# Kernel tuning notes

Hardware: AMD Instinct MI355X
Metric: run time of the kernel (lower is better)

Reference implementation:

```python
import jax, jax.numpy as jnp
import numpy as np

N_NODES = 200000
N_EDGES = 6400000
D_IN, D_HID, D_OUT = 128, 16, 172


def gcn_conv(x, edge_index, W, b, n):
    """PyG GCNConv: add self-loops, symmetric D^-1/2 A D^-1/2 normalization,
    linear projection, scatter-add aggregation, bias."""
    src, dst = edge_index[0], edge_index[1]
    loops = jnp.arange(n, dtype=edge_index.dtype)
    src = jnp.concatenate([src, loops])
    dst = jnp.concatenate([dst, loops])
    # in-degree with self-loops (>= 1, so rsqrt is safe)
    deg = jax.ops.segment_sum(jnp.ones_like(dst, dtype=x.dtype), dst, num_segments=n)
    dinv = jax.lax.rsqrt(deg)
    lin = x @ W  # [n, d_out]
    norm = dinv[src] * dinv[dst]  # per-edge normalization
    msg = lin[src] * norm[:, None]  # gather + scale
    out = jax.ops.segment_sum(msg, dst, num_segments=n)  # scatter-add
    return out + b


def setup_inputs() -> dict:
    key = jax.random.key(0)
    k1, k2, k3, k4, k5, k6 = jax.random.split(key, 6)
    x = jax.random.normal(k1, (N_NODES, D_IN), dtype=jnp.float32)
    edge_index = jax.random.randint(k2, (2, N_EDGES), 0, N_NODES, dtype=jnp.int64)
    W1 = jax.random.normal(k3, (D_IN, D_HID), dtype=jnp.float32) * (1.0 / np.sqrt(D_IN))
    b1 = jnp.zeros((D_HID,), dtype=jnp.float32)
    W2 = jax.random.normal(k4, (D_HID, D_OUT), dtype=jnp.float32) * (1.0 / np.sqrt(D_HID))
    b2 = jnp.zeros((D_OUT,), dtype=jnp.float32)
    return {"x": x, "edge_index": edge_index, "W1": W1, "b1": b1, "W2": W2, "b2": b2}


def reference(x, edge_index, W1, b1, W2, b2):
    n = x.shape[0]
    # CRD: GCNConv -> relu (dropout is identity in eval mode)
    h = jax.nn.relu(gcn_conv(x, edge_index, W1, b1, n))
    # CLS: GCNConv -> log_softmax over classes
    logits = gcn_conv(h, edge_index, W2, b2, n)
    return jax.nn.log_softmax(logits, axis=1)
```

## Files before the change

### kernel.cpp

```cpp
#include <hip/hip_runtime.h>
#include <hip/hip_fp16.h>

#define N_NODES 200000
#define N_EDGES 6400000
#define D_IN    128
#define D_HID   16
#define D_OUT   172

#define NS1     800
#define EPB     8000
#define SBN     98
#define SB_NODES 2048

#define O_BTOT  0
#define O_BASE  128
#define O_CNT1  256
#define O_ROW   78656
#define O_DINV  278784
#define O_COL   478784
#define O_PACK  6878784
#define O_F16A  6878784
#define O_F16B  8478784
#define O_AGG2  10078784

__global__ __launch_bounds__(256) void k_hist1(const int* __restrict__ dst,
                                               unsigned* __restrict__ counts) {
    __shared__ unsigned cnt[SBN];
    for (int i = threadIdx.x; i < SBN; i += 256) cnt[i] = 0;
    __syncthreads();
    const int* dp = dst + blockIdx.x * EPB;
    for (int i = threadIdx.x; i < EPB; i += 256)
        atomicAdd(&cnt[dp[i] >> 11], 1u);
    __syncthreads();
    unsigned* out = counts + (size_t)blockIdx.x * SBN;
    for (int i = threadIdx.x; i < SBN; i += 256) out[i] = cnt[i];
}

__global__ __launch_bounds__(256) void k_scan_col(unsigned* __restrict__ counts,
                                                  unsigned* __restrict__ btot) {
    __shared__ unsigned arr[NS1];
    int b = blockIdx.x;
    for (int i = threadIdx.x; i < NS1; i += 256)
        arr[i] = counts[(size_t)i * SBN + b];
    __syncthreads();
    if (threadIdx.x < 64) {
        int l = threadIdx.x;
        int lo = l * 13, hi = min(lo + 13, NS1);
        unsigned sum = 0;
        for (int i = lo; i < hi; ++i) sum += arr[i];
        unsigned incl = sum;
#pragma unroll
        for (int o = 1; o < 64; o <<= 1) {
            unsigned tmp = __shfl_up(incl, o);
            if (l >= o) incl += tmp;
        }
        if (l == 63) btot[b] = incl;
        unsigned run = incl - sum;
        for (int i = lo; i < hi; ++i) { unsigned v = arr[i]; arr[i] = run; run += v; }
    }
    __syncthreads();
    for (int i = threadIdx.x; i < NS1; i += 256)
        counts[(size_t)i * SBN + b] = arr[i];
}

__global__ __launch_bounds__(64) void k_scan_base(const unsigned* __restrict__ btot,
                                                  unsigned* __restrict__ base) {
    int l = threadIdx.x;
    int lo = l * 2, hi = min(lo + 2, SBN);
    unsigned sum = 0;
    for (int i = lo; i < hi; ++i) sum += btot[i];
    unsigned incl = sum;
#pragma unroll
    for (int o = 1; o < 64; o <<= 1) {
        unsigned tmp = __shfl_up(incl, o);
        if (l >= o) incl += tmp;
    }
    unsigned run = incl - sum;
    for (int i = lo; i < hi; ++i) { unsigned v = btot[i]; base[i] = run; run += v; }
    if (l == 63) base[SBN] = incl;
}

__global__ __launch_bounds__(256) void k_scatter1(const int* __restrict__ src,
                                                  const int* __restrict__ dst,
                                                  const unsigned* __restrict__ counts,
                                                  const unsigned* __restrict__ base,
                                                  unsigned* __restrict__ packed) {
    __shared__ unsigned off[SBN];
    const unsigned* crow = counts + (size_t)blockIdx.x * SBN;
    for (int i = threadIdx.x; i < SBN; i += 256) off[i] = base[i] + crow[i];
    __syncthreads();
    const int* sp = src + blockIdx.x * EPB;
    const int* dp = dst + blockIdx.x * EPB;
    for (int i = threadIdx.x; i < EPB; i += 256) {
        int s = sp[i], d = dp[i];
        unsigned slot = atomicAdd(&off[d >> 11], 1u);
        packed[slot] = ((unsigned)(d & (SB_NODES - 1)) << 18) | (unsigned)s;
    }
}

__global__ __launch_bounds__(1024) void k_csr(const unsigned* __restrict__ packed,
                                              const unsigned* __restrict__ base,
                                              int* __restrict__ rowptr,
                                              float* __restrict__ dinv,
                                              int* __restrict__ col) {
    __shared__ unsigned cnt[SB_NODES];
    __shared__ unsigned off[SB_NODES];
    __shared__ unsigned wsum[16];
    int t = threadIdx.x, sb = blockIdx.x;
    unsigned beg = base[sb], end = base[sb + 1];
    cnt[t] = 0; cnt[t + 1024] = 0;
    __syncthreads();
    for (unsigned i = beg + t; i < end; i += 1024)
        atomicAdd(&cnt[packed[i] >> 18], 1u);
    __syncthreads();
    unsigned e0 = cnt[2 * t], e1 = cnt[2 * t + 1], s = e0 + e1;
    int lane = t & 63, wid = t >> 6;
    unsigned incl = s;
#pragma unroll
    for (int o = 1; o < 64; o <<= 1) {
        unsigned tmp = __shfl_up(incl, o);
        if (lane >= o) incl += tmp;
    }
    if (lane == 63) wsum[wid] = incl;
    __syncthreads();
    unsigned wbase = 0;
    for (int w = 0; w < wid; ++w) wbase += wsum[w];
    unsigned ex = wbase + incl - s;
    off[2 * t]     = ex;
    off[2 * t + 1] = ex + e0;
    int n0 = sb * SB_NODES + 2 * t;
    if (n0     <= N_NODES) rowptr[n0]     = (int)(beg + ex);
    if (n0 + 1 <= N_NODES) rowptr[n0 + 1] = (int)(beg + ex + e0);
    if (n0     <  N_NODES) dinv[n0]       = rsqrtf((float)(e0 + 1));
    if (n0 + 1 <  N_NODES) dinv[n0 + 1]   = rsqrtf((float)(e1 + 1));
    __syncthreads();
    for (unsigned i = beg + t; i < end; i += 1024) {
        unsigned p = packed[i];
        unsigned slot = atomicAdd(&off[p >> 18], 1u);
        col[beg + slot] = (int)(p & 0x3FFFFu);
    }
}

__global__ __launch_bounds__(256) void k_lin1(const float* __restrict__ x,
                                              const float* __restrict__ W1,
                                              const float* __restrict__ dinv,
                                              __half* __restrict__ lin) {
    __shared__ float sW[D_IN * D_HID];
    for (int t = threadIdx.x; t < D_IN * D_HID; t += 256) sW[t] = W1[t];
    __syncthreads();

    int g  = threadIdx.x & 3;
    int nl = threadIdx.x >> 2;
    int n  = blockIdx.x * 64 + nl;

    float acc[16];
#pragma unroll
    for (int j = 0; j < 16; ++j) acc[j] = 0.f;

    const float4* xr = (const float4*)(x + (size_t)n * D_IN + g * 32);
#pragma unroll
    for (int i = 0; i < 8; ++i) {
        float4 xv = xr[i];
        int k = g * 32 + i * 4;
#pragma unroll
        for (int j = 0; j < 16; ++j) {
            acc[j] += xv.x * sW[(k + 0) * 16 + j] + xv.y * sW[(k + 1) * 16 + j]
                    + xv.z * sW[(k + 2) * 16 + j] + xv.w * sW[(k + 3) * 16 + j];
        }
    }
#pragma unroll
    for (int j = 0; j < 16; ++j) {
        acc[j] += __shfl_xor(acc[j], 1);
        acc[j] += __shfl_xor(acc[j], 2);
    }
    float di = dinv[n];
    ushort4 pk;
    pk.x = __half_as_ushort(__float2half(acc[g * 4 + 0] * di));
    pk.y = __half_as_ushort(__float2half(acc[g * 4 + 1] * di));
    pk.z = __half_as_ushort(__float2half(acc[g * 4 + 2] * di));
    pk.w = __half_as_ushort(__float2half(acc[g * 4 + 3] * di));
    *(ushort4*)(lin + (size_t)n * 16 + g * 4) = pk;
}

template <int MODE>
__global__ __launch_bounds__(256) void k_gather(const int* __restrict__ rowptr,
                                                const int* __restrict__ col,
                                                const float* __restrict__ dinv,
                                                const __half* __restrict__ fin,
                                                const float* __restrict__ bias,
                                                void* __restrict__ outv) {
    int t = threadIdx.x;
    int n = blockIdx.x * 16 + (t >> 4);
    int lane = t & 15;
    int beg = rowptr[n], end = rowptr[n + 1];
    float a0 = __half2float(fin[n * 16 + lane]);
    float a1 = 0.f, a2 = 0.f, a3 = 0.f, a4 = 0.f, a5 = 0.f, a6 = 0.f, a7 = 0.f;
    int i = beg;
    for (; i + 8 <= end; i += 8) {
        int s0 = col[i + 0], s1 = col[i + 1], s2 = col[i + 2], s3 = col[i + 3];
        int s4 = col[i + 4], s5 = col[i + 5], s6 = col[i + 6], s7 = col[i + 7];
        float f0 = __half2float(fin[s0 * 16 + lane]);
        float f1 = __half2float(fin[s1 * 16 + lane]);
        float f2 = __half2float(fin[s2 * 16 + lane]);
        float f3 = __half2float(fin[s3 * 16 + lane]);
        float f4 = __half2float(fin[s4 * 16 + lane]);
        float f5 = __half2float(fin[s5 * 16 + lane]);
        float f6 = __half2float(fin[s6 * 16 + lane]);
        float f7 = __half2float(fin[s7 * 16 + lane]);
        a0 += f0; a1 += f1; a2 += f2; a3 += f3;
        a4 += f4; a5 += f5; a6 += f6; a7 += f7;
    }
    for (; i < end; ++i) a0 += __half2float(fin[col[i] * 16 + lane]);
    float acc = ((a0 + a1) + (a2 + a3)) + ((a4 + a5) + (a6 + a7));
    float dd = dinv[n];
    float v = acc * dd;
    if (MODE) {
        v = fmaxf(v + bias[lane], 0.f) * dd;
        ((__half*)outv)[n * 16 + lane] = __float2half(v);
    } else {
        ((float*)outv)[n * 16 + lane] = v;
    }
}

__global__ __launch_bounds__(256) void k_out(const float* __restrict__ agg2,
                                             const float* __restrict__ W2,
                                             const float* __restrict__ b2,
                                             float* __restrict__ out) {
    __shared__ float sWt[D_OUT * D_HID];
    __shared__ float sb[D_OUT];
    __shared__ float sl[64 * D_OUT];
    __shared__ float sls[64];
    int t = threadIdx.x;
    for (int m = t; m < D_OUT * D_HID; m += 256)
        sWt[m] = W2[(m & 15) * D_OUT + (m >> 4)];
    for (int m = t; m < D_OUT; m += 256) sb[m] = b2[m];
    __syncthreads();

    int nl = t >> 2, q = t & 3;
    int n  = blockIdx.x * 64 + nl;
    const float4* ar = (const float4*)(agg2 + (size_t)n * 16);
    float4 a0 = ar[0], a1 = ar[1], a2 = ar[2], a3 = ar[3];
    float a[16] = {a0.x, a0.y, a0.z, a0.w, a1.x, a1.y, a1.z, a1.w,
                   a2.x, a2.y, a2.z, a2.w, a3.x, a3.y, a3.z, a3.w};

    float mloc = -INFINITY;
    float* srow = sl + nl * D_OUT;
#pragma unroll 4
    for (int i = 0; i < 43; ++i) {
        int c = q + 4 * i;
        const float4* wr = (const float4*)(sWt + c * 16);
        float4 w0 = wr[0], w1 = wr[1], w2 = wr[2], w3 = wr[3];
        float l = sb[c];
        l += a[0]  * w0.x + a[1]  * w0.y + a[2]  * w0.z + a[3]  * w0.w;
        l += a[4]  * w1.x + a[5]  * w1.y + a[6]  * w1.z + a[7]  * w1.w;
        l += a[8]  * w2.x + a[9]  * w2.y + a[10] * w2.z + a[11] * w2.w;
        l += a[12] * w3.x + a[13] * w3.y + a[14] * w3.z + a[15] * w3.w;
        srow[c] = l;
        mloc = fmaxf(mloc, l);
    }
    mloc = fmaxf(mloc, __shfl_xor(mloc, 1));
    mloc = fmaxf(mloc, __shfl_xor(mloc, 2));
    float sloc = 0.f;
#pragma unroll 4
    for (int i = 0; i < 43; ++i) sloc += __expf(srow[q + 4 * i] - mloc);
    sloc += __shfl_xor(sloc, 1);
    sloc += __shfl_xor(sloc, 2);
    if (q == 0) sls[nl] = mloc + __logf(sloc);
    __syncthreads();

    const float4* sl4 = (const float4*)sl;
    float4* ob = (float4*)(out + (size_t)blockIdx.x * 64 * D_OUT);
    for (int jj = t; jj < 64 * D_OUT / 4; jj += 256) {
        float4 v = sl4[jj];
        float ls = sls[jj / 43];
        v.x -= ls; v.y -= ls; v.z -= ls; v.w -= ls;
        ob[jj] = v;
    }
}

extern "C" void kernel_launch(void* const* d_in, const int* in_sizes, int n_in,
                              void* d_out, int out_size, void* d_ws, size_t ws_size,
                              hipStream_t stream) {
    const float* x     = (const float*)d_in[0];
    const int*   edges = (const int*)d_in[1];
    const float* W1    = (const float*)d_in[2];
    const float* b1    = (const float*)d_in[3];
    const float* W2    = (const float*)d_in[4];
    const float* b2    = (const float*)d_in[5];
    float*       out   = (float*)d_out;

    const int* src = edges;
    const int* dst = edges + N_EDGES;

    unsigned* ws     = (unsigned*)d_ws;
    unsigned* btot   = ws + O_BTOT;
    unsigned* base   = ws + O_BASE;
    unsigned* counts = ws + O_CNT1;
    int*      rowptr = (int*)(ws + O_ROW);
    float*    dinv   = (float*)(ws + O_DINV);
    int*      col    = (int*)(ws + O_COL);
    unsigned* packed = ws + O_PACK;
    __half*   f16a   = (__half*)(ws + O_F16A);
    __half*   f16b   = (__half*)(ws + O_F16B);
    float*    agg2   = (float*)(ws + O_AGG2);

    k_hist1    <<<NS1, 256, 0, stream>>>(dst, counts);
    k_scan_col <<<SBN, 256, 0, stream>>>(counts, btot);
    k_scan_base<<<1,    64, 0, stream>>>(btot, base);
    k_scatter1 <<<NS1, 256, 0, stream>>>(src, dst, counts, base, packed);
    k_csr      <<<SBN, 1024, 0, stream>>>(packed, base, rowptr, dinv, col);

    k_lin1     <<<N_NODES / 64, 256, 0, stream>>>(x, W1, dinv, f16a);
    k_gather<1><<<N_NODES / 16, 256, 0, stream>>>(rowptr, col, dinv, f16a, b1, f16b);

    k_gather<0><<<N_NODES / 16, 256, 0, stream>>>(rowptr, col, dinv, f16b, b1, agg2);
    k_out      <<<N_NODES / 64, 256, 0, stream>>>(agg2, W2, b2, out);
}
```

Before: 447.0 us.

## Quantize gathered features to int8 with global scale and shrink CSR superblocks

Adds per-layer global abs-max tracking and a quantization pass that converts the fp16 node features to int8 with a single scale. The gather kernels then read 4-byte uchar4 chunks, split each node's edges across four sub-lanes, and reduce with shuffles. The change is meant to halve the bytes moved by the random-access gathers. Separately, the CSR build switches to 512-node superblocks with 256-thread blocks and a new workspace layout. The int8 quantization with one global scale loses a lot of precision and may exceed the accuracy tolerance. The extra quant kernels add launches and memory passes.

New measurement: 542.2 us. +21.3%, slower.

```diff
diff --git a/kernel.cpp b/kernel.cpp
--- a/kernel.cpp
+++ b/kernel.cpp
@@ -9,19 +9,22 @@
 
 #define NS1     800
 #define EPB     8000
-#define SBN     98
-#define SB_NODES 2048
+#define SBN     391
+#define SB_NODES 512
 
 #define O_BTOT  0
-#define O_BASE  128
-#define O_CNT1  256
-#define O_ROW   78656
-#define O_DINV  278784
-#define O_COL   478784
-#define O_PACK  6878784
-#define O_F16A  6878784
-#define O_F16B  8478784
-#define O_AGG2  10078784
+#define O_BASE  512
+#define O_SMAX  960
+#define O_CNT1  1024
+#define O_COL   1024
+#define O_ROW   6401024
+#define O_DINV  6601088
+#define O_PACK  6801088
+#define O_F16A  6801088
+#define O_Q8A   8401088
+#define O_F16B  9201088
+#define O_Q8B   10801088
+#define O_AGG2  6801088
 
 __global__ __launch_bounds__(256) void k_hist1(const int* __restrict__ dst,
                                                unsigned* __restrict__ counts) {
@@ -30,7 +33,7 @@
     __syncthreads();
     const int* dp = dst + blockIdx.x * EPB;
     for (int i = threadIdx.x; i < EPB; i += 256)
-        atomicAdd(&cnt[dp[i] >> 11], 1u);
+        atomicAdd(&cnt[dp[i] >> 9], 1u);
     __syncthreads();
     unsigned* out = counts + (size_t)blockIdx.x * SBN;
     for (int i = threadIdx.x; i < SBN; i += 256) out[i] = cnt[i];
@@ -64,9 +67,11 @@
 }
 
 __global__ __launch_bounds__(64) void k_scan_base(const unsigned* __restrict__ btot,
-                                                  unsigned* __restrict__ base) {
+                                                  unsigned* __restrict__ base,
+                                                  unsigned* __restrict__ smax) {
     int l = threadIdx.x;
-    int lo = l * 2, hi = min(lo + 2, SBN);
+    if (l < 2) smax[l] = 0;
+    int lo = l * 7, hi = min(lo + 7, SBN);
     unsigned sum = 0;
     for (int i = lo; i < hi; ++i) sum += btot[i];
     unsigned incl = sum;
@@ -93,24 +98,24 @@
     const int* dp = dst + blockIdx.x * EPB;
     for (int i = threadIdx.x; i < EPB; i += 256) {
         int s = sp[i], d = dp[i];
-        unsigned slot = atomicAdd(&off[d >> 11], 1u);
+        unsigned slot = atomicAdd(&off[d >> 9], 1u);
         packed[slot] = ((unsigned)(d & (SB_NODES - 1)) << 18) | (unsigned)s;
     }
 }
 
-__global__ __launch_bounds__(1024) void k_csr(const unsigned* __restrict__ packed,
-                                              const unsigned* __restrict__ base,
-                                              int* __restrict__ rowptr,
-                                              float* __restrict__ dinv,
-                                              int* __restrict__ col) {
+__global__ __launch_bounds__(256) void k_csr(const unsigned* __restrict__ packed,
+                                             const unsigned* __restrict__ base,
+                                             int* __restrict__ rowptr,
+                                             float* __restrict__ dinv,
+                                             int* __restrict__ col) {
     __shared__ unsigned cnt[SB_NODES];
     __shared__ unsigned off[SB_NODES];
-    __shared__ unsigned wsum[16];
+    __shared__ unsigned wsum[4];
     int t = threadIdx.x, sb = blockIdx.x;
     unsigned beg = base[sb], end = base[sb + 1];
-    cnt[t] = 0; cnt[t + 1024] = 0;
-    __syncthreads();
-    for (unsigned i = beg + t; i < end; i += 1024)
+    cnt[t] = 0; cnt[t + 256] = 0;
+    __syncthreads();
+    for (unsigned i = beg + t; i < end; i += 256)
         atomicAdd(&cnt[packed[i] >> 18], 1u);
     __syncthreads();
     unsigned e0 = cnt[2 * t], e1 = cnt[2 * t + 1], s = e0 + e1;
@@ -134,7 +139,7 @@
     if (n0     <  N_NODES) dinv[n0]       = rsqrtf((float)(e0 + 1));
     if (n0 + 1 <  N_NODES) dinv[n0 + 1]   = rsqrtf((float)(e1 + 1));
     __syncthreads();
-    for (unsigned i = beg + t; i < end; i += 1024) {
+    for (unsigned i = beg + t; i < end; i += 256) {
         unsigned p = packed[i];
         unsigned slot = atomicAdd(&off[p >> 18], 1u);
         col[beg + slot] = (int)(p & 0x3FFFFu);
@@ -144,8 +149,11 @@
 __global__ __launch_bounds__(256) void k_lin1(const float* __restrict__ x,
                                               const float* __restrict__ W1,
                                               const float* __restrict__ dinv,
-                                              __half* __restrict__ lin) {
+                                              __half* __restrict__ lin,
+                                              unsigned* __restrict__ smax0) {
     __shared__ float sW[D_IN * D_HID];
+    __shared__ unsigned lmax;
+    if (threadIdx.x == 0) lmax = 0;
     for (int t = threadIdx.x; t < D_IN * D_HID; t += 256) sW[t] = W1[t];
     __syncthreads();
 
@@ -174,51 +182,106 @@
         acc[j] += __shfl_xor(acc[j], 2);
     }
     float di = dinv[n];
+    float v0 = acc[g * 4 + 0] * di, v1 = acc[g * 4 + 1] * di;
+    float v2 = acc[g * 4 + 2] * di, v3 = acc[g * 4 + 3] * di;
     ushort4 pk;
-    pk.x = __half_as_ushort(__float2half(acc[g * 4 + 0] * di));
-    pk.y = __half_as_ushort(__float2half(acc[g * 4 + 1] * di));
-    pk.z = __half_as_ushort(__float2half(acc[g * 4 + 2] * di));
-    pk.w = __half_as_ushort(__float2half(acc[g * 4 + 3] * di));
+    pk.x = __half_as_ushort(__float2half(v0));
+    pk.y = __half_as_ushort(__float2half(v1));
+    pk.z = __half_as_ushort(__float2half(v2));
+    pk.w = __half_as_ushort(__float2half(v3));
     *(ushort4*)(lin + (size_t)n * 16 + g * 4) = pk;
-}
-
+    float m = fmaxf(fmaxf(fabsf(v0), fabsf(v1)), fmaxf(fabsf(v2), fabsf(v3)));
+    atomicMax(&lmax, __float_as_uint(m));
+    __syncthreads();
+    if (threadIdx.x == 0) atomicMax(smax0, lmax);
+}
+
+__global__ __launch_bounds__(256) void k_quant(const __half2* __restrict__ hin,
+                                               const unsigned* __restrict__ smax,
+                                               uchar4* __restrict__ q8) {
+    int i = blockIdx.x * 256 + threadIdx.x;
+    float mx = __uint_as_float(*smax);
+    float rs = mx > 0.f ? 127.0f / mx : 0.f;
+    __half2 p0 = hin[2 * i], p1 = hin[2 * i + 1];
+    float2 f0 = __half22float2(p0), f1 = __half22float2(p1);
+    int q0 = min(max(__float2int_rn(f0.x * rs), -127), 127);
+    int q1 = min(max(__float2int_rn(f0.y * rs), -127), 127);
+    int q2 = min(max(__float2int_rn(f1.x * rs), -127), 127);
+    int q3 = min(max(__float2int_rn(f1.y * rs), -127), 127);
+    uchar4 o;
+    o.x = (unsigned char)q0; o.y = (unsigned char)q1;
+    o.z = (unsigned char)q2; o.w = (unsigned char)q3;
+    q8[i] = o;
+}
+
+#define DQ(u) make_float4((float)(signed char)(u).x, (float)(signed char)(u).y, \
+                          (float)(signed char)(u).z, (float)(signed char)(u).w)
 template <int MODE>
-__global__ __launch_bounds__(256) void k_gather(const int* __restrict__ rowptr,
-                                                const int* __restrict__ col,
-                                                const float* __restrict__ dinv,
-                                                const __half* __restrict__ fin,
-                                                const float* __restrict__ bias,
-                                                void* __restrict__ outv) {
+__global__ __launch_bounds__(256) void k_gather8(const int* __restrict__ rowptr,
+                                                 const int* __restrict__ col,
+                                                 const float* __restrict__ dinv,
+                                                 const uchar4* __restrict__ q8,
+                                                 const unsigned* __restrict__ sin,
+                                                 unsigned* __restrict__ sout,
+                                                 const float* __restrict__ bias,
+                                                 void* __restrict__ outv) {
+    __shared__ unsigned lmax;
     int t = threadIdx.x;
+    if (MODE) {
+        if (t == 0) lmax = 0;
+        __syncthreads();
+    }
     int n = blockIdx.x * 16 + (t >> 4);
-    int lane = t & 15;
+    int sub = t & 15, ep = sub >> 2, fb = sub & 3;
     int beg = rowptr[n], end = rowptr[n + 1];
-    float a0 = __half2float(fin[n * 16 + lane]);
-    float a1 = 0.f, a2 = 0.f, a3 = 0.f, a4 = 0.f, a5 = 0.f, a6 = 0.f, a7 = 0.f;
-    int i = beg;
-    for (; i + 8 <= end; i += 8) {
-        int s0 = col[i + 0], s1 = col[i + 1], s2 = col[i + 2], s3 = col[i + 3];
-        int s4 = col[i + 4], s5 = col[i + 5], s6 = col[i + 6], s7 = col[i + 7];
-        float f0 = __half2float(fin[s0 * 16 + lane]);
-        float f1 = __half2float(fin[s1 * 16 + lane]);
-        float f2 = __half2float(fin[s2 * 16 + lane]);
-        float f3 = __half2float(fin[s3 * 16 + lane]);
-        float f4 = __half2float(fin[s4 * 16 + lane]);
-        float f5 = __half2float(fin[s5 * 16 + lane]);
-        float f6 = __half2float(fin[s6 * 16 + lane]);
-        float f7 = __half2float(fin[s7 * 16 + lane]);
-        a0 += f0; a1 += f1; a2 += f2; a3 += f3;
-        a4 += f4; a5 += f5; a6 += f6; a7 += f7;
-    }
-    for (; i < end; ++i) a0 += __half2float(fin[col[i] * 16 + lane]);
-    float acc = ((a0 + a1) + (a2 + a3)) + ((a4 + a5) + (a6 + a7));
+    float ax = 0, ay = 0, az = 0, aw = 0, bx = 0, by = 0, bz = 0, bw = 0;
+    if (ep == 0) {
+        uchar4 u = q8[n * 4 + fb];
+        float4 f = DQ(u);
+        ax = f.x; ay = f.y; az = f.z; aw = f.w;
+    }
+    int i = beg + ep;
+    for (; i + 4 < end; i += 8) {
+        int s0 = col[i], s1 = col[i + 4];
+        uchar4 u0 = q8[s0 * 4 + fb], u1 = q8[s1 * 4 + fb];
+        float4 f0 = DQ(u0), f1 = DQ(u1);
+        ax += f0.x; ay += f0.y; az += f0.z; aw += f0.w;
+        bx += f1.x; by += f1.y; bz += f1.z; bw += f1.w;
+    }
+    if (i < end) {
+        uchar4 u = q8[col[i] * 4 + fb];
+        float4 f = DQ(u);
+        ax += f.x; ay += f.y; az += f.z; aw += f.w;
+    }
+    float vx = ax + bx, vy = ay + by, vz = az + bz, vw = aw + bw;
+    vx += __shfl_xor(vx, 4); vx += __shfl_xor(vx, 8);
+    vy += __shfl_xor(vy, 4); vy += __shfl_xor(vy, 8);
+    vz += __shfl_xor(vz, 4); vz += __shfl_xor(vz, 8);
+    vw += __shfl_xor(vw, 4); vw += __shfl_xor(vw, 8);
     float dd = dinv[n];
-    float v = acc * dd;
+    float sc = __uint_as_float(*sin) * (1.0f / 127.0f) * dd;
+    vx *= sc; vy *= sc; vz *= sc; vw *= sc;
     if (MODE) {
-        v = fmaxf(v + bias[lane], 0.f) * dd;
-        ((__half*)outv)[n * 16 + lane] = __float2half(v);
+        float4 b4 = ((const float4*)bias)[fb];
+        vx = fmaxf(vx + b4.x, 0.f) * dd;
+        vy = fmaxf(vy + b4.y, 0.f) * dd;
+        vz = fmaxf(vz + b4.z, 0.f) * dd;
+        vw = fmaxf(vw + b4.w, 0.f) * dd;
+        if (ep == 0) {
+            ushort4 o;
+            o.x = __half_as_ushort(__float2half(vx));
+            o.y = __half_as_ushort(__float2half(vy));
+            o.z = __half_as_ushort(__float2half(vz));
+            o.w = __half_as_ushort(__float2half(vw));
+            ((ushort4*)outv)[n * 4 + fb] = o;
+            float m = fmaxf(fmaxf(vx, vy), fmaxf(vz, vw));
+            atomicMax(&lmax, __float_as_uint(m));
+        }
+        __syncthreads();
+        if (t == 0) atomicMax(sout, lmax);
     } else {
-        ((float*)outv)[n * 16 + lane] = v;
+        if (ep == 0)
+            ((float4*)outv)[n * 4 + fb] = make_float4(vx, vy, vz, vw);
     }
 }
 
@@ -295,24 +358,30 @@
     unsigned* ws     = (unsigned*)d_ws;
     unsigned* btot   = ws + O_BTOT;
     unsigned* base   = ws + O_BASE;
+    unsigned* smax   = ws + O_SMAX;
     unsigned* counts = ws + O_CNT1;
+    int*      col    = (int*)(ws + O_COL);
     int*      rowptr = (int*)(ws + O_ROW);
     float*    dinv   = (float*)(ws + O_DINV);
-    int*      col    = (int*)(ws + O_COL);
     unsigned* packed = ws + O_PACK;
     __half*   f16a   = (__half*)(ws + O_F16A);
+    uchar4*   q8a    = (uchar4*)(ws + O_Q8A);
     __half*   f16b   = (__half*)(ws + O_F16B);
+    uchar4*   q8b    = (uchar4*)(ws + O_Q8B);
     float*    agg2   = (float*)(ws + O_AGG2);
 
     k_hist1    <<<NS1, 256, 0, stream>>>(dst, counts);
     k_scan_col <<<SBN, 256, 0, stream>>>(counts, btot);
-    k_scan_base<<<1,    64, 0, stream>>>(btot, base);
+    k_scan_base<<<1,    64, 0, stream>>>(btot, base, smax);
     k_scatter1 <<<NS1, 256, 0, stream>>>(src, dst, counts, base, packed);
-    k_csr      <<<SBN, 1024, 0, stream>>>(packed, base, rowptr, dinv, col);
-
-    k_lin1     <<<N_NODES / 64, 256, 0, stream>>>(x, W1, dinv, f16a);
-    k_gather<1><<<N_NODES / 16, 256, 0, stream>>>(rowptr, col, dinv, f16a, b1, f16b);
-
-    k_gather<0><<<N_NODES / 16, 256, 0, stream>>>(rowptr, col, dinv, f16b, b1, agg2);
+    k_csr      <<<SBN, 256, 0, stream>>>(packed, base, rowptr, dinv, col);
+
+    k_lin1     <<<N_NODES / 64, 256, 0, stream>>>(x, W1, dinv, f16a, smax);
+    k_quant    <<<3125, 256, 0, stream>>>((const __half2*)f16a, smax, q8a);
+    k_gather8<1><<<N_NODES / 16, 256, 0, stream>>>(rowptr, col, dinv, q8a,
+                                                   smax, smax + 1, b1, f16b);
+    k_quant    <<<3125, 256, 0, stream>>>((const __half2*)f16b, smax + 1, q8b);
+    k_gather8<0><<<N_NODES / 16, 256, 0, stream>>>(rowptr, col, dinv, q8b,
+                                                   smax + 1, nullptr, b1, agg2);
     k_out      <<<N_NODES / 64, 256, 0, stream>>>(agg2, W2, b2, out);
 }
```
